# Performance work log

Measured on AMD Instinct MI355X. Metric: run time of the kernel, lower is better.

The kernel has to match this reference:

```python
import jax, jax.numpy as jnp
import numpy as np

TOP_K = 2


def setup_inputs() -> dict:
    key = jax.random.key(0)
    ks = jax.random.split(key, 8)
    B, S, D, I, E = 4, 2048, 1024, 2048, 8
    scale = 0.02
    return {
        "hidden_states": jax.random.normal(ks[0], (B, S, D), dtype=jnp.float32),
        "router_w": jax.random.normal(ks[1], (D, E), dtype=jnp.float32) * scale,
        "router_b": jnp.zeros((E,), dtype=jnp.float32),
        "gate_w": jax.random.normal(ks[2], (E, D, I), dtype=jnp.float32) * scale,
        "gate_b": jnp.zeros((E, I), dtype=jnp.float32),
        "up_w": jax.random.normal(ks[3], (E, D, I), dtype=jnp.float32) * scale,
        "up_b": jnp.zeros((E, I), dtype=jnp.float32),
        "down_w": jax.random.normal(ks[4], (E, I, D), dtype=jnp.float32) * scale,
        "down_b": jnp.zeros((E, D), dtype=jnp.float32),
    }


def reference(hidden_states, router_w, router_b, gate_w, gate_b, up_w, up_b, down_w, down_b):
    B, S, D = hidden_states.shape
    E = router_w.shape[1]
    x = hidden_states.reshape(-1, D)  # [T, D]
    T = x.shape[0]

    # Router: softmax over experts, then top-k selection + renormalization
    logits = x @ router_w + router_b              # [T, E]
    probs = jax.nn.softmax(logits, axis=-1)       # [T, E]
    top_v, top_i = jax.lax.top_k(probs, TOP_K)    # [T, K]
    top_v = top_v / jnp.sum(top_v, axis=-1, keepdims=True)

    # Scatter renormalized probs to dense [T, E] combine weights (top-k indices are distinct)
    weights = jnp.zeros((T, E), dtype=x.dtype).at[jnp.arange(T)[:, None], top_i].set(top_v)

    # Dense expert SwiGLU: compute all experts, weighted combine (faithful math)
    gate = jnp.einsum('td,edi->eti', x, gate_w) + gate_b[:, None, :]   # [E, T, I]
    up = jnp.einsum('td,edi->eti', x, up_w) + up_b[:, None, :]         # [E, T, I]
    h = jax.nn.silu(gate) * up                                          # [E, T, I]
    expert_out = jnp.einsum('eti,eid->etd', h, down_w) + down_b[:, None, :]  # [E, T, D]

    y = jnp.einsum('te,etd->td', weights, expert_out)                   # [T, D]
    return y.reshape(B, S, D)
```

## Files before the change

### kernel.cpp

```cpp
#include <hip/hip_runtime.h>

#define T_TOK 8192
#define DDIM 1024
#define IDIM 2048
#define NEXP 8

typedef short bf16x8 __attribute__((ext_vector_type(8)));
typedef float f32x4 __attribute__((ext_vector_type(4)));

__device__ __forceinline__ unsigned short f2bf(float f) {
  union { float f; unsigned int u; } v; v.f = f;
  unsigned int r = v.u + 0x7fffu + ((v.u >> 16) & 1u);
  return (unsigned short)(r >> 16);
}
__device__ __forceinline__ float bf2f(unsigned short u) {
  union { unsigned int u; float f; } v; v.u = (unsigned int)u << 16;
  return v.f;
}

typedef const __attribute__((address_space(1))) void* gas_t;
typedef __attribute__((address_space(3))) void* las_t;
__device__ __forceinline__ void async_copy16(void* lds, const void* g) {
  __builtin_amdgcn_global_load_lds((gas_t)g, (las_t)lds, 16, 0, 0);
}

__global__ __launch_bounds__(256) void convert_kernel(const float* __restrict__ x,
                                                      ushort* __restrict__ xb, int n4) {
  int i = blockIdx.x * 256 + threadIdx.x;
  if (i >= n4) return;
  float4 v = ((const float4*)x)[i];
  ushort4 o;
  o.x = f2bf(v.x); o.y = f2bf(v.y); o.z = f2bf(v.z); o.w = f2bf(v.w);
  ((ushort4*)xb)[i] = o;
}

__global__ __launch_bounds__(256) void tconv_kernel(
    const float* __restrict__ src, ushort* __restrict__ dst, int R, int C,
    int sel, int interleave, size_t srcEStride, size_t dstEStride) {
  __shared__ ushort lt[64 * 72];
  const int e = blockIdx.z;
  const float* s = src + (size_t)e * srcEStride;
  ushort* d = dst + (size_t)e * dstEStride;
  const int c0 = blockIdx.x * 64, r0 = blockIdx.y * 64;
  const int t = threadIdx.x;
  const int tr = t >> 2;
  const int tc = (t & 3) * 16;
  const float* sp = s + (size_t)(r0 + tr) * C + c0 + tc;
  float4 v0 = ((const float4*)sp)[0];
  float4 v1 = ((const float4*)sp)[1];
  float4 v2 = ((const float4*)sp)[2];
  float4 v3 = ((const float4*)sp)[3];
#pragma unroll
  for (int j = 0; j < 4; ++j) lt[(tc + j) * 72 + tr]      = f2bf(((const float*)&v0)[j]);
#pragma unroll
  for (int j = 0; j < 4; ++j) lt[(tc + 4 + j) * 72 + tr]  = f2bf(((const float*)&v1)[j]);
#pragma unroll
  for (int j = 0; j < 4; ++j) lt[(tc + 8 + j) * 72 + tr]  = f2bf(((const float*)&v2)[j]);
#pragma unroll
  for (int j = 0; j < 4; ++j) lt[(tc + 12 + j) * 72 + tr] = f2bf(((const float*)&v3)[j]);
  __syncthreads();
  const int cr = t >> 2;
  const int seg = (t & 3) * 16;
  const int ci = c0 + cr;
  const int drow = interleave ? ((ci >> 6) * 128 + sel * 64 + (ci & 63)) : ci;
  uint4 o0 = *(const uint4*)&lt[cr * 72 + seg];
  uint4 o1 = *(const uint4*)&lt[cr * 72 + seg + 8];
  ushort* dp = d + (size_t)drow * R + r0 + seg;
  *(uint4*)dp = o0;
  *(uint4*)(dp + 8) = o1;
}

__global__ __launch_bounds__(256) void router_kernel(
    const float* __restrict__ x, const float* __restrict__ rw, const float* __restrict__ rb,
    int* __restrict__ cnt, int* __restrict__ lists, float* __restrict__ wts,
    int* __restrict__ pexp) {
  __shared__ int tokE[128];
  __shared__ int loc[128];
  __shared__ int hist[NEXP];
  __shared__ int base[NEXP];
  const int tid = threadIdx.x;
  const int w = tid >> 6, lane = tid & 63;
  if (tid < NEXP) hist[tid] = 0;
  __syncthreads();

#pragma unroll 1
  for (int tt = 0; tt < 16; ++tt) {
    const int token = blockIdx.x * 64 + w * 16 + tt;
    float acc[NEXP];
#pragma unroll
    for (int e = 0; e < NEXP; ++e) acc[e] = 0.f;
    const float* xr = x + (size_t)token * DDIM;
#pragma unroll
    for (int j = 0; j < DDIM / 64; ++j) {
      int d = j * 64 + lane;
      float xv = xr[d];
      const float4* wp = (const float4*)(rw + d * NEXP);
      float4 w0 = wp[0], w1 = wp[1];
      acc[0] += xv * w0.x; acc[1] += xv * w0.y; acc[2] += xv * w0.z; acc[3] += xv * w0.w;
      acc[4] += xv * w1.x; acc[5] += xv * w1.y; acc[6] += xv * w1.z; acc[7] += xv * w1.w;
    }
#pragma unroll
    for (int e = 0; e < NEXP; ++e) {
      float v = acc[e];
      for (int off = 32; off > 0; off >>= 1) v += __shfl_xor(v, off, 64);
      acc[e] = v;
    }
    if (lane == 0) {
      float l[NEXP];
#pragma unroll
      for (int e = 0; e < NEXP; ++e) l[e] = acc[e] + rb[e];
      int i0 = 0; float b0 = l[0];
#pragma unroll
      for (int e = 1; e < NEXP; ++e) if (l[e] > b0) { b0 = l[e]; i0 = e; }
      int i1 = -1; float b1 = -3.0e38f;
#pragma unroll
      for (int e = 0; e < NEXP; ++e) if (e != i0 && l[e] > b1) { b1 = l[e]; i1 = e; }
      float e1 = expf(b1 - b0);
      float inv = 1.f / (1.f + e1);
      wts[token * 2 + 0] = inv;
      wts[token * 2 + 1] = e1 * inv;
      pexp[token * 2 + 0] = i0;
      pexp[token * 2 + 1] = i1;
      const int k = (w * 16 + tt) * 2;
      tokE[k] = i0;
      tokE[k + 1] = i1;
      loc[k] = atomicAdd(&hist[i0], 1);
      loc[k + 1] = atomicAdd(&hist[i1], 1);
    }
  }
  __syncthreads();
  if (tid < NEXP) base[tid] = atomicAdd(&cnt[tid], hist[tid]);
  __syncthreads();
  if (tid < 128) {
    const int e = tokE[tid];
    const int token = blockIdx.x * 64 + (tid >> 1);
    lists[e * T_TOK + base[e] + loc[tid]] = token * 2 + (tid & 1);
  }
}

__global__ __launch_bounds__(256, 2) void gemm1_kernel(
    const ushort* __restrict__ xb, const ushort* __restrict__ wcat,
    const float* __restrict__ gate_b, const float* __restrict__ up_b,
    const int* __restrict__ lists, const int* __restrict__ cnt,
    ushort* __restrict__ hbuf) {
  const int e = blockIdx.z;
  const int ce = cnt[e];
  const int p = blockIdx.x + (blockIdx.y << 6);
  const int l = (p & 7) * 256 + (p >> 3);
  const int m0 = (l & 63) * 128;
  const int by = l >> 6;
  if (m0 >= ce) return;

  __shared__ __align__(16) ushort smem[2 * 128 * 64];
  __shared__ int rowinfo[128];
  ushort* As = smem;
  ushort* Bs = smem + 128 * 64;

  const int tid = threadIdx.x;
  if (tid < 128) {
    int slot = m0 + tid;
    rowinfo[tid] = lists[e * T_TOK + (slot < ce ? slot : 0)];
  }
  __syncthreads();

  const int w = tid >> 6, lane = tid & 63;
  const int fm = lane & 15, fq = lane >> 4;
  const int waveM = w >> 1, waveN = w & 1;
  const int lr = lane >> 3;
  const int lchunk = ((lane & 7) ^ lr) * 8;

  const ushort* wcatE = wcat + (size_t)e * 4096 * 1024;
  const ushort* aG[4]; const ushort* bG[4];
  ushort* aL[4]; ushort* bL[4];
#pragma unroll
  for (int j = 0; j < 4; ++j) {
    int rl = 32 * w + 8 * j + lr;
    aG[j] = xb + (size_t)(rowinfo[rl] >> 1) * DDIM + lchunk;
    bG[j] = wcatE + (size_t)(128 * by + rl) * DDIM + lchunk;
    aL[j] = As + (32 * w + 8 * j) * 64;
    bL[j] = Bs + (32 * w + 8 * j) * 64;
  }

  f32x4 acc[4][4];
  const f32x4 zero4 = {0.f, 0.f, 0.f, 0.f};
#pragma unroll
  for (int i = 0; i < 4; ++i)
#pragma unroll
    for (int j = 0; j < 4; ++j) acc[i][j] = zero4;

#pragma unroll 1
  for (int kt = 0; kt < DDIM / 64; ++kt) {
    __syncthreads();
#pragma unroll
    for (int j = 0; j < 4; ++j) {
      async_copy16(aL[j], aG[j] + kt * 64);
      async_copy16(bL[j], bG[j] + kt * 64);
    }
    __syncthreads();
#pragma unroll
    for (int ks = 0; ks < 2; ++ks) {
      bf16x8 af[4], bfr[4];
#pragma unroll
      for (int mf = 0; mf < 4; ++mf) {
        int row = 64 * waveM + 16 * mf + fm;
        af[mf] = *(const bf16x8*)&As[row * 64 + (((ks * 4 + fq) ^ (fm & 7)) * 8)];
      }
#pragma unroll
      for (int nf = 0; nf < 4; ++nf) {
        int row = 64 * waveN + 16 * nf + fm;
        bfr[nf] = *(const bf16x8*)&Bs[row * 64 + (((ks * 4 + fq) ^ (fm & 7)) * 8)];
      }
#pragma unroll
      for (int mf = 0; mf < 4; ++mf)
#pragma unroll
        for (int nf = 0; nf < 4; ++nf)
          acc[mf][nf] = __builtin_amdgcn_mfma_f32_16x16x32_bf16(af[mf], bfr[nf], acc[mf][nf], 0, 0, 0);
    }
  }

  __syncthreads();
  float* uld = (float*)smem;
  if (waveN == 1) {
#pragma unroll
    for (int mf = 0; mf < 4; ++mf)
#pragma unroll
      for (int nf = 0; nf < 4; ++nf)
#pragma unroll
        for (int r = 0; r < 4; ++r)
          uld[(64 * waveM + 16 * mf + 4 * fq + r) * 64 + 16 * nf + fm] = acc[mf][nf][r];
  }
  __syncthreads();
  if (waveN == 0) {
#pragma unroll
    for (int mf = 0; mf < 4; ++mf) {
#pragma unroll
      for (int r = 0; r < 4; ++r) {
        const int row = 64 * waveM + 16 * mf + 4 * fq + r;
        if (m0 + row < ce) {
          const int packed = rowinfo[row];
#pragma unroll
          for (int nf = 0; nf < 4; ++nf) {
            const int col = 64 * by + 16 * nf + fm;
            float g = acc[mf][nf][r] + gate_b[e * IDIM + col];
            float u = uld[row * 64 + 16 * nf + fm] + up_b[e * IDIM + col];
            float h = g * (1.f / (1.f + __expf(-g))) * u;
            hbuf[(size_t)packed * IDIM + col] = f2bf(h);
          }
        }
      }
    }
  }
}

__global__ __launch_bounds__(256, 2) void gemm2_kernel(
    const ushort* __restrict__ hbuf, const ushort* __restrict__ downT,
    const int* __restrict__ lists, const int* __restrict__ cnt,
    ushort* __restrict__ cbuf) {
  const int e = blockIdx.z;
  const int ce = cnt[e];
  const int p = blockIdx.x + (blockIdx.y << 6);
  const int l = (p & 7) * 64 + (p >> 3);
  const int m0 = (l & 63) * 128;
  const int by = l >> 6;
  if (m0 >= ce) return;

  __shared__ __align__(16) ushort smem[2 * 128 * 64];
  __shared__ int rowinfo[128];
  ushort* As = smem;
  ushort* Bs = smem + 128 * 64;

  const int tid = threadIdx.x;
  if (tid < 128) {
    int slot = m0 + tid;
    rowinfo[tid] = lists[e * T_TOK + (slot < ce ? slot : 0)];
  }
  __syncthreads();

  const int w = tid >> 6, lane = tid & 63;
  const int fm = lane & 15, fq = lane >> 4;
  const int waveM = w >> 1, waveN = w & 1;
  const int lr = lane >> 3;
  const int lchunk = ((lane & 7) ^ lr) * 8;

  const ushort* downE = downT + (size_t)e * DDIM * IDIM;
  const ushort* aG[4]; const ushort* bG[4];
  ushort* aL[4]; ushort* bL[4];
#pragma unroll
  for (int j = 0; j < 4; ++j) {
    int rl = 32 * w + 8 * j + lr;
    aG[j] = hbuf + (size_t)rowinfo[rl] * IDIM + lchunk;
    bG[j] = downE + (size_t)(128 * by + rl) * IDIM + lchunk;
    aL[j] = As + (32 * w + 8 * j) * 64;
    bL[j] = Bs + (32 * w + 8 * j) * 64;
  }

  f32x4 acc[4][4];
  const f32x4 zero4 = {0.f, 0.f, 0.f, 0.f};
#pragma unroll
  for (int i = 0; i < 4; ++i)
#pragma unroll
    for (int j = 0; j < 4; ++j) acc[i][j] = zero4;

#pragma unroll 1
  for (int kt = 0; kt < IDIM / 64; ++kt) {
    __syncthreads();
#pragma unroll
    for (int j = 0; j < 4; ++j) {
      async_copy16(aL[j], aG[j] + kt * 64);
      async_copy16(bL[j], bG[j] + kt * 64);
    }
    __syncthreads();
#pragma unroll
    for (int ks = 0; ks < 2; ++ks) {
      bf16x8 af[4], bfr[4];
#pragma unroll
      for (int mf = 0; mf < 4; ++mf) {
        int row = 64 * waveM + 16 * mf + fm;
        af[mf] = *(const bf16x8*)&As[row * 64 + (((ks * 4 + fq) ^ (fm & 7)) * 8)];
      }
#pragma unroll
      for (int nf = 0; nf < 4; ++nf) {
        int row = 64 * waveN + 16 * nf + fm;
        bfr[nf] = *(const bf16x8*)&Bs[row * 64 + (((ks * 4 + fq) ^ (fm & 7)) * 8)];
      }
#pragma unroll
      for (int mf = 0; mf < 4; ++mf)
#pragma unroll
        for (int nf = 0; nf < 4; ++nf)
          acc[mf][nf] = __builtin_amdgcn_mfma_f32_16x16x32_bf16(af[mf], bfr[nf], acc[mf][nf], 0, 0, 0);
    }
  }

#pragma unroll
  for (int mf = 0; mf < 4; ++mf) {
#pragma unroll
    for (int r = 0; r < 4; ++r) {
      const int row = 64 * waveM + 16 * mf + 4 * fq + r;
      if (m0 + row < ce) {
        const int packed = rowinfo[row];
        ushort* crow = cbuf + (size_t)packed * DDIM + 128 * by + 64 * waveN;
#pragma unroll
        for (int nf = 0; nf < 4; ++nf)
          crow[16 * nf + fm] = f2bf(acc[mf][nf][r]);
      }
    }
  }
}

__global__ __launch_bounds__(256) void combine_kernel(
    const ushort* __restrict__ cbuf, const float* __restrict__ down_b,
    const int* __restrict__ pexp, const float* __restrict__ wts,
    float* __restrict__ out) {
  const int i = blockIdx.x * 256 + threadIdx.x;
  const int token = i >> 7;
  const int seg = (i & 127) * 8;
  const float w0 = wts[token * 2], w1 = wts[token * 2 + 1];
  const int e0 = pexp[token * 2], e1 = pexp[token * 2 + 1];
  const ushort* c0 = cbuf + (size_t)(token * 2) * DDIM + seg;
  const ushort* c1 = c0 + DDIM;
  const float* b0 = down_b + e0 * DDIM + seg;
  const float* b1 = down_b + e1 * DDIM + seg;
  ushort4 v0a = ((const ushort4*)c0)[0], v0b = ((const ushort4*)c0)[1];
  ushort4 v1a = ((const ushort4*)c1)[0], v1b = ((const ushort4*)c1)[1];
  float4 ba0 = ((const float4*)b0)[0], bb0 = ((const float4*)b0)[1];
  float4 ba1 = ((const float4*)b1)[0], bb1 = ((const float4*)b1)[1];
  float4 o0, o1;
  o0.x = w0 * (bf2f(v0a.x) + ba0.x) + w1 * (bf2f(v1a.x) + ba1.x);
  o0.y = w0 * (bf2f(v0a.y) + ba0.y) + w1 * (bf2f(v1a.y) + ba1.y);
  o0.z = w0 * (bf2f(v0a.z) + ba0.z) + w1 * (bf2f(v1a.z) + ba1.z);
  o0.w = w0 * (bf2f(v0a.w) + ba0.w) + w1 * (bf2f(v1a.w) + ba1.w);
  o1.x = w0 * (bf2f(v0b.x) + bb0.x) + w1 * (bf2f(v1b.x) + bb1.x);
  o1.y = w0 * (bf2f(v0b.y) + bb0.y) + w1 * (bf2f(v1b.y) + bb1.y);
  o1.z = w0 * (bf2f(v0b.z) + bb0.z) + w1 * (bf2f(v1b.z) + bb1.z);
  o1.w = w0 * (bf2f(v0b.w) + bb0.w) + w1 * (bf2f(v1b.w) + bb1.w);
  float* op = out + (size_t)token * DDIM + seg;
  ((float4*)op)[0] = o0;
  ((float4*)op)[1] = o1;
}

extern "C" void kernel_launch(void* const* d_in, const int* in_sizes, int n_in,
                              void* d_out, int out_size, void* d_ws, size_t ws_size,
                              hipStream_t stream) {
  const float* x = (const float*)d_in[0];
  const float* rw = (const float*)d_in[1];
  const float* rb = (const float*)d_in[2];
  const float* gw = (const float*)d_in[3];
  const float* gb = (const float*)d_in[4];
  const float* uw = (const float*)d_in[5];
  const float* ub = (const float*)d_in[6];
  const float* dw = (const float*)d_in[7];
  const float* db = (const float*)d_in[8];
  float* out = (float*)d_out;

  char* ws = (char*)d_ws;
  ushort* xb    = (ushort*)(ws);
  ushort* hbuf  = (ushort*)(ws + (16ull << 20));
  ushort* wcat  = (ushort*)(ws + (80ull << 20));
  ushort* cbuf  = wcat;
  ushort* downT = (ushort*)(ws + (144ull << 20));
  float*  wts   = (float*) (ws + (176ull << 20));
  int*    lists = (int*)   (ws + (176ull << 20) + 65536);
  int*    cnt   = (int*)   (ws + (176ull << 20) + 65536 + 262144);
  int*    pexp  = (int*)   (ws + (176ull << 20) + 65536 + 262144 + 4096);

  hipMemsetAsync(cnt, 0, NEXP * sizeof(int), stream);

  convert_kernel<<<(T_TOK * DDIM / 4 + 255) / 256, 256, 0, stream>>>(x, xb, T_TOK * DDIM / 4);
  router_kernel<<<T_TOK / 64, 256, 0, stream>>>(x, rw, rb, cnt, lists, wts, pexp);
  tconv_kernel<<<dim3(IDIM / 64, DDIM / 64, NEXP), 256, 0, stream>>>(
      gw, wcat, DDIM, IDIM, 0, 1, (size_t)DDIM * IDIM, (size_t)2 * IDIM * DDIM);
  tconv_kernel<<<dim3(IDIM / 64, DDIM / 64, NEXP), 256, 0, stream>>>(
      uw, wcat, DDIM, IDIM, 1, 1, (size_t)DDIM * IDIM, (size_t)2 * IDIM * DDIM);
  tconv_kernel<<<dim3(DDIM / 64, IDIM / 64, NEXP), 256, 0, stream>>>(
      dw, downT, IDIM, DDIM, 0, 0, (size_t)IDIM * DDIM, (size_t)DDIM * IDIM);

  gemm1_kernel<<<dim3(T_TOK / 128, IDIM / 64, NEXP), 256, 0, stream>>>(
      xb, wcat, gb, ub, lists, cnt, hbuf);
  gemm2_kernel<<<dim3(T_TOK / 128, DDIM / 128, NEXP), 256, 0, stream>>>(
      hbuf, downT, lists, cnt, cbuf);
  combine_kernel<<<T_TOK * DDIM / 8 / 256, 256, 0, stream>>>(cbuf, db, pexp, wts, out);
}
```

Measured before the change: 578.1 us.

## Widen expert GEMM tiles to 128x256 and fuse bf16 conversion into router

Both grouped GEMMs move from 128x128 to 128x256 output tiles, with each wave holding a 4x8 accumulator grid. In gemm1 each wave's tile now contains matching gate and up columns, so SwiGLU is applied straight from registers instead of passing through an LDS exchange. The standalone fp32-to-bf16 conversion kernel is removed and the router writes the bf16 copy of x while it reads x anyway. The larger tiles reuse each A row more and drop a launch and a pass over x, but they double accumulator registers and raise LDS use, which may cut occupancy. They also halve the number of blocks on a ragged expert workload.

```diff
diff --git a/kernel.cpp b/kernel.cpp
--- a/kernel.cpp
+++ b/kernel.cpp
@@ -22,16 +22,6 @@
 typedef __attribute__((address_space(3))) void* las_t;
 __device__ __forceinline__ void async_copy16(void* lds, const void* g) {
   __builtin_amdgcn_global_load_lds((gas_t)g, (las_t)lds, 16, 0, 0);
-}
-
-__global__ __launch_bounds__(256) void convert_kernel(const float* __restrict__ x,
-                                                      ushort* __restrict__ xb, int n4) {
-  int i = blockIdx.x * 256 + threadIdx.x;
-  if (i >= n4) return;
-  float4 v = ((const float4*)x)[i];
-  ushort4 o;
-  o.x = f2bf(v.x); o.y = f2bf(v.y); o.z = f2bf(v.z); o.w = f2bf(v.w);
-  ((ushort4*)xb)[i] = o;
 }
 
 __global__ __launch_bounds__(256) void tconv_kernel(
@@ -73,7 +63,7 @@
 __global__ __launch_bounds__(256) void router_kernel(
     const float* __restrict__ x, const float* __restrict__ rw, const float* __restrict__ rb,
     int* __restrict__ cnt, int* __restrict__ lists, float* __restrict__ wts,
-    int* __restrict__ pexp) {
+    int* __restrict__ pexp, ushort* __restrict__ xb) {
   __shared__ int tokE[128];
   __shared__ int loc[128];
   __shared__ int hist[NEXP];
@@ -90,10 +80,12 @@
 #pragma unroll
     for (int e = 0; e < NEXP; ++e) acc[e] = 0.f;
     const float* xr = x + (size_t)token * DDIM;
+    ushort* xbr = xb + (size_t)token * DDIM;
 #pragma unroll
     for (int j = 0; j < DDIM / 64; ++j) {
       int d = j * 64 + lane;
       float xv = xr[d];
+      xbr[d] = f2bf(xv);
       const float4* wp = (const float4*)(rw + d * NEXP);
       float4 w0 = wp[0], w1 = wp[1];
       acc[0] += xv * w0.x; acc[1] += xv * w0.y; acc[2] += xv * w0.z; acc[3] += xv * w0.w;
@@ -146,12 +138,12 @@
   const int e = blockIdx.z;
   const int ce = cnt[e];
   const int p = blockIdx.x + (blockIdx.y << 6);
-  const int l = (p & 7) * 256 + (p >> 3);
+  const int l = (p & 7) * 128 + (p >> 3);
   const int m0 = (l & 63) * 128;
   const int by = l >> 6;
   if (m0 >= ce) return;
 
-  __shared__ __align__(16) ushort smem[2 * 128 * 64];
+  __shared__ __align__(16) ushort smem[128 * 64 + 256 * 64];
   __shared__ int rowinfo[128];
   ushort* As = smem;
   ushort* Bs = smem + 128 * 64;
@@ -170,82 +162,72 @@
   const int lchunk = ((lane & 7) ^ lr) * 8;
 
   const ushort* wcatE = wcat + (size_t)e * 4096 * 1024;
-  const ushort* aG[4]; const ushort* bG[4];
-  ushort* aL[4]; ushort* bL[4];
+  const ushort* aG[4]; const ushort* bG[8];
+  ushort* aL[4]; ushort* bL[8];
 #pragma unroll
   for (int j = 0; j < 4; ++j) {
     int rl = 32 * w + 8 * j + lr;
     aG[j] = xb + (size_t)(rowinfo[rl] >> 1) * DDIM + lchunk;
-    bG[j] = wcatE + (size_t)(128 * by + rl) * DDIM + lchunk;
     aL[j] = As + (32 * w + 8 * j) * 64;
-    bL[j] = Bs + (32 * w + 8 * j) * 64;
-  }
-
-  f32x4 acc[4][4];
+  }
+#pragma unroll
+  for (int j = 0; j < 8; ++j) {
+    int rl = 64 * w + 8 * j + lr;
+    bG[j] = wcatE + (size_t)(256 * by + rl) * DDIM + lchunk;
+    bL[j] = Bs + (64 * w + 8 * j) * 64;
+  }
+
+  f32x4 acc[4][8];
   const f32x4 zero4 = {0.f, 0.f, 0.f, 0.f};
 #pragma unroll
   for (int i = 0; i < 4; ++i)
 #pragma unroll
-    for (int j = 0; j < 4; ++j) acc[i][j] = zero4;
+    for (int j = 0; j < 8; ++j) acc[i][j] = zero4;
 
 #pragma unroll 1
   for (int kt = 0; kt < DDIM / 64; ++kt) {
     __syncthreads();
 #pragma unroll
-    for (int j = 0; j < 4; ++j) {
-      async_copy16(aL[j], aG[j] + kt * 64);
-      async_copy16(bL[j], bG[j] + kt * 64);
-    }
+    for (int j = 0; j < 4; ++j) async_copy16(aL[j], aG[j] + kt * 64);
+#pragma unroll
+    for (int j = 0; j < 8; ++j) async_copy16(bL[j], bG[j] + kt * 64);
     __syncthreads();
 #pragma unroll
     for (int ks = 0; ks < 2; ++ks) {
-      bf16x8 af[4], bfr[4];
+      bf16x8 af[4], bfr[8];
 #pragma unroll
       for (int mf = 0; mf < 4; ++mf) {
         int row = 64 * waveM + 16 * mf + fm;
         af[mf] = *(const bf16x8*)&As[row * 64 + (((ks * 4 + fq) ^ (fm & 7)) * 8)];
       }
 #pragma unroll
-      for (int nf = 0; nf < 4; ++nf) {
-        int row = 64 * waveN + 16 * nf + fm;
+      for (int nf = 0; nf < 8; ++nf) {
+        int row = 128 * waveN + 16 * nf + fm;
         bfr[nf] = *(const bf16x8*)&Bs[row * 64 + (((ks * 4 + fq) ^ (fm & 7)) * 8)];
       }
 #pragma unroll
       for (int mf = 0; mf < 4; ++mf)
 #pragma unroll
-        for (int nf = 0; nf < 4; ++nf)
+        for (int nf = 0; nf < 8; ++nf)
           acc[mf][nf] = __builtin_amdgcn_mfma_f32_16x16x32_bf16(af[mf], bfr[nf], acc[mf][nf], 0, 0, 0);
     }
   }
 
-  __syncthreads();
-  float* uld = (float*)smem;
-  if (waveN == 1) {
-#pragma unroll
-    for (int mf = 0; mf < 4; ++mf)
-#pragma unroll
-      for (int nf = 0; nf < 4; ++nf)
-#pragma unroll
-        for (int r = 0; r < 4; ++r)
-          uld[(64 * waveM + 16 * mf + 4 * fq + r) * 64 + 16 * nf + fm] = acc[mf][nf][r];
-  }
-  __syncthreads();
-  if (waveN == 0) {
-#pragma unroll
-    for (int mf = 0; mf < 4; ++mf) {
-#pragma unroll
-      for (int r = 0; r < 4; ++r) {
-        const int row = 64 * waveM + 16 * mf + 4 * fq + r;
-        if (m0 + row < ce) {
-          const int packed = rowinfo[row];
-#pragma unroll
-          for (int nf = 0; nf < 4; ++nf) {
-            const int col = 64 * by + 16 * nf + fm;
-            float g = acc[mf][nf][r] + gate_b[e * IDIM + col];
-            float u = uld[row * 64 + 16 * nf + fm] + up_b[e * IDIM + col];
-            float h = g * (1.f / (1.f + __expf(-g))) * u;
-            hbuf[(size_t)packed * IDIM + col] = f2bf(h);
-          }
+  const int g_group = 2 * by + waveN;
+#pragma unroll
+  for (int mf = 0; mf < 4; ++mf) {
+#pragma unroll
+    for (int r = 0; r < 4; ++r) {
+      const int row = 64 * waveM + 16 * mf + 4 * fq + r;
+      if (m0 + row < ce) {
+        const int packed = rowinfo[row];
+#pragma unroll
+        for (int nf = 0; nf < 4; ++nf) {
+          const int col = 64 * g_group + 16 * nf + fm;
+          float g = acc[mf][nf][r] + gate_b[e * IDIM + col];
+          float u = acc[mf][nf + 4][r] + up_b[e * IDIM + col];
+          float h = g * (1.f / (1.f + __expf(-g))) * u;
+          hbuf[(size_t)packed * IDIM + col] = f2bf(h);
         }
       }
     }
@@ -259,12 +241,12 @@
   const int e = blockIdx.z;
   const int ce = cnt[e];
   const int p = blockIdx.x + (blockIdx.y << 6);
-  const int l = (p & 7) * 64 + (p >> 3);
+  const int l = (p & 7) * 32 + (p >> 3);
   const int m0 = (l & 63) * 128;
   const int by = l >> 6;
   if (m0 >= ce) return;
 
-  __shared__ __align__(16) ushort smem[2 * 128 * 64];
+  __shared__ __align__(16) ushort smem[128 * 64 + 256 * 64];
   __shared__ int rowinfo[128];
   ushort* As = smem;
   ushort* Bs = smem + 128 * 64;
@@ -283,50 +265,53 @@
   const int lchunk = ((lane & 7) ^ lr) * 8;
 
   const ushort* downE = downT + (size_t)e * DDIM * IDIM;
-  const ushort* aG[4]; const ushort* bG[4];
-  ushort* aL[4]; ushort* bL[4];
+  const ushort* aG[4]; const ushort* bG[8];
+  ushort* aL[4]; ushort* bL[8];
 #pragma unroll
   for (int j = 0; j < 4; ++j) {
     int rl = 32 * w + 8 * j + lr;
     aG[j] = hbuf + (size_t)rowinfo[rl] * IDIM + lchunk;
-    bG[j] = downE + (size_t)(128 * by + rl) * IDIM + lchunk;
     aL[j] = As + (32 * w + 8 * j) * 64;
-    bL[j] = Bs + (32 * w + 8 * j) * 64;
-  }
-
-  f32x4 acc[4][4];
+  }
+#pragma unroll
+  for (int j = 0; j < 8; ++j) {
+    int rl = 64 * w + 8 * j + lr;
+    bG[j] = downE + (size_t)(256 * by + rl) * IDIM + lchunk;
+    bL[j] = Bs + (64 * w + 8 * j) * 64;
+  }
+
+  f32x4 acc[4][8];
   const f32x4 zero4 = {0.f, 0.f, 0.f, 0.f};
 #pragma unroll
   for (int i = 0; i < 4; ++i)
 #pragma unroll
-    for (int j = 0; j < 4; ++j) acc[i][j] = zero4;
+    for (int j = 0; j < 8; ++j) acc[i][j] = zero4;
 
 #pragma unroll 1
   for (int kt = 0; kt < IDIM / 64; ++kt) {
     __syncthreads();
 #pragma unroll
-    for (int j = 0; j < 4; ++j) {
-      async_copy16(aL[j], aG[j] + kt * 64);
-      async_copy16(bL[j], bG[j] + kt * 64);
-    }
+    for (int j = 0; j < 4; ++j) async_copy16(aL[j], aG[j] + kt * 64);
+#pragma unroll
+    for (int j = 0; j < 8; ++j) async_copy16(bL[j], bG[j] + kt * 64);
     __syncthreads();
 #pragma unroll
     for (int ks = 0; ks < 2; ++ks) {
-      bf16x8 af[4], bfr[4];
+      bf16x8 af[4], bfr[8];
 #pragma unroll
       for (int mf = 0; mf < 4; ++mf) {
         int row = 64 * waveM + 16 * mf + fm;
         af[mf] = *(const bf16x8*)&As[row * 64 + (((ks * 4 + fq) ^ (fm & 7)) * 8)];
       }
 #pragma unroll
-      for (int nf = 0; nf < 4; ++nf) {
-        int row = 64 * waveN + 16 * nf + fm;
+      for (int nf = 0; nf < 8; ++nf) {
+        int row = 128 * waveN + 16 * nf + fm;
         bfr[nf] = *(const bf16x8*)&Bs[row * 64 + (((ks * 4 + fq) ^ (fm & 7)) * 8)];
       }
 #pragma unroll
       for (int mf = 0; mf < 4; ++mf)
 #pragma unroll
-        for (int nf = 0; nf < 4; ++nf)
+        for (int nf = 0; nf < 8; ++nf)
           acc[mf][nf] = __builtin_amdgcn_mfma_f32_16x16x32_bf16(af[mf], bfr[nf], acc[mf][nf], 0, 0, 0);
     }
   }
@@ -338,9 +323,9 @@
       const int row = 64 * waveM + 16 * mf + 4 * fq + r;
       if (m0 + row < ce) {
         const int packed = rowinfo[row];
-        ushort* crow = cbuf + (size_t)packed * DDIM + 128 * by + 64 * waveN;
-#pragma unroll
-        for (int nf = 0; nf < 4; ++nf)
+        ushort* crow = cbuf + (size_t)packed * DDIM + 256 * by + 128 * waveN;
+#pragma unroll
+        for (int nf = 0; nf < 8; ++nf)
           crow[16 * nf + fm] = f2bf(acc[mf][nf][r]);
       }
     }
@@ -405,8 +390,7 @@
 
   hipMemsetAsync(cnt, 0, NEXP * sizeof(int), stream);
 
-  convert_kernel<<<(T_TOK * DDIM / 4 + 255) / 256, 256, 0, stream>>>(x, xb, T_TOK * DDIM / 4);
-  router_kernel<<<T_TOK / 64, 256, 0, stream>>>(x, rw, rb, cnt, lists, wts, pexp);
+  router_kernel<<<T_TOK / 64, 256, 0, stream>>>(x, rw, rb, cnt, lists, wts, pexp, xb);
   tconv_kernel<<<dim3(IDIM / 64, DDIM / 64, NEXP), 256, 0, stream>>>(
       gw, wcat, DDIM, IDIM, 0, 1, (size_t)DDIM * IDIM, (size_t)2 * IDIM * DDIM);
   tconv_kernel<<<dim3(IDIM / 64, DDIM / 64, NEXP), 256, 0, stream>>>(
@@ -414,9 +398,9 @@
   tconv_kernel<<<dim3(DDIM / 64, IDIM / 64, NEXP), 256, 0, stream>>>(
       dw, downT, IDIM, DDIM, 0, 0, (size_t)IDIM * DDIM, (size_t)DDIM * IDIM);
 
-  gemm1_kernel<<<dim3(T_TOK / 128, IDIM / 64, NEXP), 256, 0, stream>>>(
+  gemm1_kernel<<<dim3(T_TOK / 128, IDIM / 128, NEXP), 256, 0, stream>>>(
       xb, wcat, gb, ub, lists, cnt, hbuf);
-  gemm2_kernel<<<dim3(T_TOK / 128, DDIM / 128, NEXP), 256, 0, stream>>>(
+  gemm2_kernel<<<dim3(T_TOK / 128, DDIM / 256, NEXP), 256, 0, stream>>>(
       hbuf, downT, lists, cnt, cbuf);
   combine_kernel<<<T_TOK * DDIM / 8 / 256, 256, 0, stream>>>(cbuf, db, pexp, wts, out);
 }
```

Measured after the change: 603.4 us. 4.4% more time.
